# Kernel optimization log

Hardware: AMD Instinct MI355X
Metric: run time of the kernel (lower is better)

Reference implementation:

```python
import jax, jax.numpy as jnp
import numpy as np

B, N, K, C = 2, 4096, 2048, 16
DSPAN, E, H, V = 2048, 300, 512, 100000
WEIGHT = 1.0


def setup_inputs() -> dict:
    key = jax.random.key(0)
    ks = jax.random.split(key, 10)
    return {
        "cand_span_vecs": jax.random.normal(ks[0], (B, N, DSPAN), jnp.float32),
        "targets_all": jax.random.uniform(ks[1], (B, N, C), jnp.float32),
        "entity_emb": jax.random.normal(ks[2], (V, E), jnp.float32) * 0.02,
        "W1": jax.random.normal(ks[3], (DSPAN + E, H), jnp.float32) * 0.02,
        "b1": jnp.zeros((H,), jnp.float32),
        "W2": jax.random.normal(ks[4], (H, 1), jnp.float32) * 0.02,
        "b2": jnp.zeros((1,), jnp.float32),
        "linker_indices_hoi": jax.random.randint(ks[5], (B, K), 0, N, jnp.int64),
        "candidates_all": jax.random.randint(ks[6], (B, N, C), 0, V, jnp.int64),
        "candidate_lengths_all": jax.random.randint(ks[7], (B, N), 0, C + 1, jnp.int64),
    }


def reference(cand_span_vecs, targets_all, entity_emb, W1, b1, W2, b2,
              linker_indices_hoi, candidates_all, candidate_lengths_all):
    idx = linker_indices_hoi  # [B, K]
    # batched_index_select over the span axis
    candidates = jnp.take_along_axis(candidates_all, idx[:, :, None], axis=1)      # [B,K,C]
    cand_lens = jnp.take_along_axis(candidate_lengths_all, idx, axis=1)            # [B,K]
    targets = jnp.take_along_axis(targets_all, idx[:, :, None], axis=1)            # [B,K,C]
    linker_vecs = jnp.take_along_axis(cand_span_vecs, idx[:, :, None], axis=1)     # [B,K,Dspan]
    # entity embedding lookup
    candidate_vecs = entity_emb[candidates]                                        # [B,K,C,E]
    # expand span vecs over candidate axis and concat
    span_exp = jnp.broadcast_to(linker_vecs[:, :, None, :],
                                (linker_vecs.shape[0], linker_vecs.shape[1],
                                 candidate_vecs.shape[2], linker_vecs.shape[2]))
    vecs = jnp.concatenate([span_exp, candidate_vecs], axis=-1)                    # [B,K,C,Dspan+E]
    # FFNN: Linear -> ReLU -> (dropout is identity in eval) -> Linear
    h = jax.nn.relu(jnp.einsum('bkcd,dh->bkch', vecs, W1) + b1)
    scores = (jnp.einsum('bkch,ho->bkco', h, W2) + b2)[..., 0]                     # [B,K,C]
    # candidate mask: valid where position < candidate_length
    mask = (jnp.arange(scores.shape[-1]) < cand_lens[:, :, None]).astype(scores.dtype)
    # BCEWithLogits (reduction='none'): softplus(x) - x*t
    bce = jax.nn.softplus(scores) - scores * targets
    obj = (mask * bce).sum() * WEIGHT
    return obj
```

## Files before the change

### kernel.cpp

```cpp
#include <hip/hip_runtime.h>
#include <math.h>

#define NN 4096
#define CC 16
#define DSP 2048
#define ED 300
#define HD 512

typedef __attribute__((ext_vector_type(8))) short short8;
typedef __attribute__((ext_vector_type(4))) float f32x4;

#define MFMA16(a, b, c) __builtin_amdgcn_mfma_f32_16x16x32_bf16((a), (b), (c), 0, 0, 0)

__device__ __forceinline__ unsigned short f2bf(float x) {
    unsigned u = __builtin_bit_cast(unsigned, x);
    u += 0x7FFFu + ((u >> 16) & 1u);
    return (unsigned short)(u >> 16);
}

__device__ __forceinline__ void gl_lds16(const void* g, void* l) {
    __builtin_amdgcn_global_load_lds(
        (const __attribute__((address_space(1))) unsigned*)g,
        (__attribute__((address_space(3))) unsigned*)l, 16, 0, 0);
}

__global__ __launch_bounds__(256) void prep_gather_scan(
    const float* __restrict__ W1,
    const float* __restrict__ span,
    const int*   __restrict__ lidx,
    const int*   __restrict__ clens,
    unsigned short* __restrict__ W1sT,
    unsigned short* __restrict__ w1ef,
    unsigned short* __restrict__ A16,
    int*            __restrict__ off)
{
    const int bid = blockIdx.x, tid = threadIdx.x;

    if (bid == 4432) {
        __shared__ int ls[256];
        int myl[16];
        int msum = 0;
#pragma unroll
        for (int j = 0; j < 16; ++j) {
            int bk = tid * 16 + j;
            size_t base = (size_t)(bk >> 11) * NN + lidx[bk];
            int len = clens[base];
            len = len < 0 ? 0 : (len > CC ? CC : len);
            myl[j] = len; msum += len;
        }
        ls[tid] = msum;
        __syncthreads();
        for (int d = 1; d < 256; d <<= 1) {
            int v = (tid >= d) ? ls[tid - d] : 0;
            __syncthreads();
            ls[tid] += v;
            __syncthreads();
        }
        int run = ls[tid] - msum;
#pragma unroll
        for (int j = 0; j < 16; ++j) { off[tid * 16 + j] = run; run += myl[j]; }
        if (tid == 255) off[4096] = run;
        return;
    }
    if (bid >= 336) {
        const int bk = bid - 336;
        const float* src = span + ((size_t)(bk >> 11) * NN + lidx[bk]) * DSP;
        float4 x = *(const float4*)(src + tid * 8);
        float4 y = *(const float4*)(src + tid * 8 + 4);
        unsigned short v[8] = { f2bf(x.x), f2bf(x.y), f2bf(x.z), f2bf(x.w),
                                f2bf(y.x), f2bf(y.y), f2bf(y.z), f2bf(y.w) };
        *(short8*)&A16[(size_t)bk * DSP + tid * 8] = *(short8*)v;
        return;
    }
    if (bid < 256) {
        __shared__ float t[64][65];
        const int k0 = (bid >> 3) * 64, n0 = (bid & 7) * 64;
#pragma unroll
        for (int p = 0; p < 16; ++p) {
            int flat = p * 256 + tid;
            int r = flat >> 6, c = flat & 63;
            t[r][c] = W1[(size_t)(k0 + r) * HD + n0 + c];
        }
        __syncthreads();
#pragma unroll
        for (int p = 0; p < 16; ++p) {
            int flat = p * 256 + tid;
            int c = flat >> 6, r = flat & 63;
            W1sT[(size_t)(n0 + c) * DSP + k0 + r] = f2bf(t[r][c]);
        }
    } else {
        int t0 = (bid - 256) * 256 + tid;
        int lane = t0 & 63;
        int ks = (t0 >> 6) % 10;
        int ncg = (t0 >> 6) / 10;
        int col = ncg * 16 + (lane & 15);
        int kb = ks * 32 + ((lane >> 4) << 3);
        unsigned short v[8];
#pragma unroll
        for (int j = 0; j < 8; ++j) {
            int k = kb + j;
            v[j] = (k < ED) ? f2bf(W1[(size_t)(DSP + k) * HD + col]) : (unsigned short)0;
        }
        *(short8*)&w1ef[(size_t)t0 * 8] = *(short8*)v;
    }
}

__global__ __launch_bounds__(256) void gemm_and_fill(
    const unsigned short* __restrict__ A16,
    const unsigned short* __restrict__ BT,
    const float* __restrict__ b1,
    float* __restrict__ Cout,
    const int* __restrict__ lidx,
    const int* __restrict__ cands,
    const int* __restrict__ clens,
    const int* __restrict__ off,
    int* __restrict__ compact_cand,
    int* __restrict__ compact_meta)
{
    const int tid = threadIdx.x;

    if (blockIdx.x >= 512) {
        int fb = blockIdx.x - 512;
        int item0 = (fb * 256 + tid) * 4;
#pragma unroll
        for (int q = 0; q < 4; ++q) {
            int item = item0 + q;
            int bk = item >> 4, c = item & 15;
            size_t base = (size_t)(bk >> 11) * NN + lidx[bk];
            int len = clens[base];
            len = len > CC ? CC : len;
            if (c < len) {
                int pos = off[bk] + c;
                compact_cand[pos] = cands[base * CC + c];
                compact_meta[pos] = item;
            }
        }
        return;
    }

    __shared__ __align__(16) unsigned short As[2][64 * 64];
    __shared__ __align__(16) unsigned short Bs[2][64 * 64];
    const int l = tid & 63, wid = tid >> 6;
    const int wr = (wid >> 1) * 32, wc = (wid & 1) * 32;

    const int bid = blockIdx.x;
    const int brow = ((bid & 7) * 8 + ((bid >> 3) >> 3)) * 64;
    const int bcol = (((bid >> 3) & 7)) * 64;

    const int s0 = tid, s1 = tid + 256;
    const int r0 = s0 >> 3, c0 = ((s0 & 7) ^ (r0 & 7)) * 8;
    const int r1 = s1 >> 3, c1 = ((s1 & 7) ^ (r1 & 7)) * 8;
    const unsigned short* ga0 = A16 + (size_t)(brow + r0) * DSP + c0;
    const unsigned short* ga1 = A16 + (size_t)(brow + r1) * DSP + c1;
    const unsigned short* gb0 = BT + (size_t)(bcol + r0) * DSP + c0;
    const unsigned short* gb1 = BT + (size_t)(bcol + r1) * DSP + c1;

    int offA[2][2], offB[2][2];
#pragma unroll
    for (int mf = 0; mf < 2; ++mf) {
        int row = wr + mf * 16 + (l & 15);
#pragma unroll
        for (int kk = 0; kk < 2; ++kk)
            offA[mf][kk] = row * 64 + (((kk * 4) + (l >> 4)) ^ (row & 7)) * 8;
    }
#pragma unroll
    for (int nf = 0; nf < 2; ++nf) {
        int row = wc + nf * 16 + (l & 15);
#pragma unroll
        for (int kk = 0; kk < 2; ++kk)
            offB[nf][kk] = row * 64 + (((kk * 4) + (l >> 4)) ^ (row & 7)) * 8;
    }

    f32x4 z = {0.f, 0.f, 0.f, 0.f};
    f32x4 acc[2][2] = {{z, z}, {z, z}};

    auto stage = [&](int buf, int k0) {
        gl_lds16(ga0 + k0, &As[buf][s0 * 8]);
        gl_lds16(ga1 + k0, &As[buf][s1 * 8]);
        gl_lds16(gb0 + k0, &Bs[buf][s0 * 8]);
        gl_lds16(gb1 + k0, &Bs[buf][s1 * 8]);
    };

    stage(0, 0);
    __syncthreads();
    int cur = 0;
    for (int t = 0; t < 32; ++t) {
        if (t < 31) stage(cur ^ 1, (t + 1) * 64);
        short8 am[2][2], bn[2][2];
#pragma unroll
        for (int mf = 0; mf < 2; ++mf)
#pragma unroll
            for (int kk = 0; kk < 2; ++kk)
                am[mf][kk] = *(const short8*)&As[cur][offA[mf][kk]];
#pragma unroll
        for (int nf = 0; nf < 2; ++nf)
#pragma unroll
            for (int kk = 0; kk < 2; ++kk)
                bn[nf][kk] = *(const short8*)&Bs[cur][offB[nf][kk]];
#pragma unroll
        for (int m = 0; m < 2; ++m)
#pragma unroll
            for (int n = 0; n < 2; ++n)
#pragma unroll
                for (int kk = 0; kk < 2; ++kk)
                    acc[m][n] = MFMA16(am[m][kk], bn[n][kk], acc[m][n]);
        __syncthreads();
        cur ^= 1;
    }

#pragma unroll
    for (int n = 0; n < 2; ++n) {
        int col = bcol + wc + n * 16 + (l & 15);
        float b1v = b1[col];
#pragma unroll
        for (int m = 0; m < 2; ++m) {
            int row0 = brow + wr + m * 16 + (l >> 4) * 4;
#pragma unroll
            for (int r = 0; r < 4; ++r)
                Cout[(size_t)(row0 + r) * HD + col] = acc[m][n][r] + b1v;
        }
    }
}

__global__ __launch_bounds__(512) void ent_mfma(
    const unsigned short* __restrict__ w1ef,
    const float* __restrict__ span_part,
    const float* __restrict__ emb,
    const float* __restrict__ W2,
    const float* __restrict__ b2,
    const int*   __restrict__ lidx,
    const float* __restrict__ targets,
    const int*   __restrict__ compact_cand,
    const int*   __restrict__ compact_meta,
    const int*   __restrict__ off,
    float* __restrict__ blockPartial)
{
    const int total = off[4096];
    const int bid = blockIdx.x;
    const int slotBase = bid * 128;
    const int tid = threadIdx.x;
    if (slotBase >= total) {
        if (tid == 0) blockPartial[bid] = 0.f;
        return;
    }

    __shared__ __align__(16) unsigned short As[2][8 * 64 * 8];
    __shared__ float shp[8][16][8];
    __shared__ int   meta_s[128];
    __shared__ float wred[8];
    const int wid = tid >> 6, l = tid & 63;

    if (tid < 128) {
        int slot = slotBase + tid;
        meta_s[tid] = (slot < total) ? compact_meta[slot] : -1;
    }

    const int slot_s = slotBase + wid * 16 + (l & 15);
    const int cid = (slot_s < total) ? compact_cand[slot_s] : 0;
    const float* erow = emb + (size_t)cid * ED;
    const int kb = (l >> 4) * 8;
    const int ht = wid;

    float4 lx = *(const float4*)(erow + kb);
    float4 ly = *(const float4*)(erow + kb + 4);
    {
        unsigned short v[8] = { f2bf(lx.x), f2bf(lx.y), f2bf(lx.z), f2bf(lx.w),
                                f2bf(ly.x), f2bf(ly.y), f2bf(ly.z), f2bf(ly.w) };
        *(short8*)&As[0][tid * 8] = *(short8*)v;
    }
    __syncthreads();

    f32x4 z = {0.f, 0.f, 0.f, 0.f};
    f32x4 acc[8][4];
#pragma unroll
    for (int g = 0; g < 8; ++g)
#pragma unroll
        for (int nc = 0; nc < 4; ++nc) acc[g][nc] = z;

    int cur = 0;
    for (int ks = 0; ks < 10; ++ks) {
        const bool pf = (ks < 9);
        if (pf) {
            int k = (ks + 1) * 32 + kb;
            if (k + 8 <= ED) {
                lx = *(const float4*)(erow + k);
                ly = *(const float4*)(erow + k + 4);
            } else {
                float tmp[8];
#pragma unroll
                for (int j = 0; j < 8; ++j) tmp[j] = (k + j < ED) ? erow[k + j] : 0.f;
                lx = make_float4(tmp[0], tmp[1], tmp[2], tmp[3]);
                ly = make_float4(tmp[4], tmp[5], tmp[6], tmp[7]);
            }
        }
        short8 af[8];
#pragma unroll
        for (int g = 0; g < 8; ++g)
            af[g] = *(const short8*)&As[cur][(g * 64 + l) * 8];
#pragma unroll
        for (int nc = 0; nc < 4; ++nc) {
            short8 bf = *(const short8*)&w1ef[(((size_t)(ht * 4 + nc) * 10 + ks) * 64 + l) * 8];
#pragma unroll
            for (int g = 0; g < 8; ++g)
                acc[g][nc] = MFMA16(af[g], bf, acc[g][nc]);
        }
        if (pf) {
            unsigned short v[8] = { f2bf(lx.x), f2bf(lx.y), f2bf(lx.z), f2bf(lx.w),
                                    f2bf(ly.x), f2bf(ly.y), f2bf(ly.z), f2bf(ly.w) };
            *(short8*)&As[cur ^ 1][tid * 8] = *(short8*)v;
        }
        __syncthreads();
        cur ^= 1;
    }

    float w2v[4];
#pragma unroll
    for (int nc = 0; nc < 4; ++nc) w2v[nc] = W2[ht * 64 + nc * 16 + (l & 15)];
    const int rq = (l >> 4) * 4;

#pragma unroll
    for (int g = 0; g < 8; ++g) {
        int bkR[4];
#pragma unroll
        for (int i = 0; i < 4; ++i) {
            int m = meta_s[g * 16 + rq + i];
            bkR[i] = (m >= 0) ? (m >> 4) : 0;
        }
        float s[4] = {0.f, 0.f, 0.f, 0.f};
#pragma unroll
        for (int nc = 0; nc < 4; ++nc) {
            int col = ht * 64 + nc * 16 + (l & 15);
            f32x4 a = acc[g][nc];
#pragma unroll
            for (int i = 0; i < 4; ++i) {
                float sp = span_part[(size_t)bkR[i] * HD + col];
                s[i] += fmaxf(a[i] + sp, 0.f) * w2v[nc];
            }
        }
#pragma unroll
        for (int m = 1; m < 16; m <<= 1) {
#pragma unroll
            for (int i = 0; i < 4; ++i) s[i] += __shfl_xor(s[i], m, 64);
        }
        if ((l & 15) == 0) {
#pragma unroll
            for (int i = 0; i < 4; ++i) shp[g][rq + i][ht] = s[i];
        }
    }
    __syncthreads();

    float val = 0.f;
    if (tid < 128) {
        int m = meta_s[tid];
        if (m >= 0) {
            int bk = m >> 4, c = m & 15;
            size_t base = (size_t)(bk >> 11) * NN + lidx[bk];
            const float* p = &shp[tid >> 4][tid & 15][0];
            float sc = ((p[0] + p[1]) + (p[2] + p[3])) +
                       ((p[4] + p[5]) + (p[6] + p[7])) + b2[0];
            float tg = targets[base * CC + c];
            val = fmaxf(sc, 0.f) + log1pf(expf(-fabsf(sc))) - sc * tg;
        }
    }
#pragma unroll
    for (int m = 32; m; m >>= 1) val += __shfl_xor(val, m, 64);
    if (l == 0) wred[wid] = val;
    __syncthreads();
    if (tid == 0) {
        float s = 0.f;
#pragma unroll
        for (int w = 0; w < 8; ++w) s += wred[w];
        blockPartial[bid] = s;
    }
}

__global__ __launch_bounds__(256) void final_reduce(
    const float* __restrict__ bp, float* __restrict__ out)
{
    __shared__ float red[4];
    float s = bp[threadIdx.x] + bp[threadIdx.x + 256];
#pragma unroll
    for (int m = 32; m; m >>= 1) s += __shfl_xor(s, m, 64);
    if ((threadIdx.x & 63) == 0) red[threadIdx.x >> 6] = s;
    __syncthreads();
    if (threadIdx.x == 0)
        out[0] = (red[0] + red[1]) + (red[2] + red[3]);
}

extern "C" void kernel_launch(void* const* d_in, const int* in_sizes, int n_in,
                              void* d_out, int out_size, void* d_ws, size_t ws_size,
                              hipStream_t stream) {
    const float* span    = (const float*)d_in[0];
    const float* targets = (const float*)d_in[1];
    const float* emb     = (const float*)d_in[2];
    const float* W1      = (const float*)d_in[3];
    const float* b1      = (const float*)d_in[4];
    const float* W2      = (const float*)d_in[5];
    const float* b2      = (const float*)d_in[6];
    const int*   lidx    = (const int*)d_in[7];
    const int*   cands   = (const int*)d_in[8];
    const int*   clens   = (const int*)d_in[9];

    char* ws = (char*)d_ws;
    unsigned short* W1sT      = (unsigned short*)(ws);
    unsigned short* w1ef      = (unsigned short*)(ws + 2097152);
    unsigned short* A16       = (unsigned short*)(ws + 2424832);
    float*          span_part = (float*)(ws + 19202048);
    int*            off       = (int*)(ws + 27590656);
    int*            ccand     = (int*)(ws + 27623424);
    int*            cmeta     = (int*)(ws + 27885568);
    float*          bpart     = (float*)(ws + 28147712);

    prep_gather_scan<<<4433, 256, 0, stream>>>(W1, span, lidx, clens,
                                               W1sT, w1ef, A16, off);
    gemm_and_fill<<<576, 256, 0, stream>>>(A16, W1sT, b1, span_part,
                                           lidx, cands, clens, off, ccand, cmeta);
    ent_mfma<<<512, 512, 0, stream>>>(w1ef, span_part, emb, W2, b2,
                                      lidx, targets, ccand, cmeta, off, bpart);
    final_reduce<<<1, 256, 0, stream>>>(bpart, (float*)d_out);
}
```

Before: 66.69 us.

## Fuse span gather and bf16 conversion into GEMM A-tile loads; store span_part as bf16

Drops the separate gather pass that wrote a bf16 copy of the selected span rows (A16). The GEMM now reads fp32 span rows directly through lidx, converts them to bf16 in registers and writes them into swizzled LDS, prefetching one tile ahead. The span_part output is also stored as bf16, which halves its write and gather traffic in the entity kernel. The cost is that A-tile loads no longer use the async global-to-LDS path, so conversion work adds register pressure inside the main loop, and span_part loses some precision.

```diff
diff --git a/kernel.cpp b/kernel.cpp
--- a/kernel.cpp
+++ b/kernel.cpp
@@ -18,25 +18,33 @@
     return (unsigned short)(u >> 16);
 }
 
+__device__ __forceinline__ float bf2f(unsigned short u) {
+    return __builtin_bit_cast(float, (unsigned)u << 16);
+}
+
 __device__ __forceinline__ void gl_lds16(const void* g, void* l) {
     __builtin_amdgcn_global_load_lds(
         (const __attribute__((address_space(1))) unsigned*)g,
         (__attribute__((address_space(3))) unsigned*)l, 16, 0, 0);
 }
 
-__global__ __launch_bounds__(256) void prep_gather_scan(
+__device__ __forceinline__ void pack8(unsigned short* dst, float4 a, float4 b) {
+    unsigned short v[8] = { f2bf(a.x), f2bf(a.y), f2bf(a.z), f2bf(a.w),
+                            f2bf(b.x), f2bf(b.y), f2bf(b.z), f2bf(b.w) };
+    *(short8*)dst = *(short8*)v;
+}
+
+__global__ __launch_bounds__(256) void prep_scan(
     const float* __restrict__ W1,
-    const float* __restrict__ span,
     const int*   __restrict__ lidx,
     const int*   __restrict__ clens,
     unsigned short* __restrict__ W1sT,
     unsigned short* __restrict__ w1ef,
-    unsigned short* __restrict__ A16,
     int*            __restrict__ off)
 {
     const int bid = blockIdx.x, tid = threadIdx.x;
 
-    if (bid == 4432) {
+    if (bid == 336) {
         __shared__ int ls[256];
         int myl[16];
         int msum = 0;
@@ -60,16 +68,6 @@
 #pragma unroll
         for (int j = 0; j < 16; ++j) { off[tid * 16 + j] = run; run += myl[j]; }
         if (tid == 255) off[4096] = run;
-        return;
-    }
-    if (bid >= 336) {
-        const int bk = bid - 336;
-        const float* src = span + ((size_t)(bk >> 11) * NN + lidx[bk]) * DSP;
-        float4 x = *(const float4*)(src + tid * 8);
-        float4 y = *(const float4*)(src + tid * 8 + 4);
-        unsigned short v[8] = { f2bf(x.x), f2bf(x.y), f2bf(x.z), f2bf(x.w),
-                                f2bf(y.x), f2bf(y.y), f2bf(y.z), f2bf(y.w) };
-        *(short8*)&A16[(size_t)bk * DSP + tid * 8] = *(short8*)v;
         return;
     }
     if (bid < 256) {
@@ -106,14 +104,14 @@
 }
 
 __global__ __launch_bounds__(256) void gemm_and_fill(
-    const unsigned short* __restrict__ A16,
+    const float* __restrict__ span,
     const unsigned short* __restrict__ BT,
     const float* __restrict__ b1,
-    float* __restrict__ Cout,
     const int* __restrict__ lidx,
     const int* __restrict__ cands,
     const int* __restrict__ clens,
     const int* __restrict__ off,
+    unsigned short* __restrict__ Cout,
     int* __restrict__ compact_cand,
     int* __restrict__ compact_meta)
 {
@@ -148,12 +146,18 @@
     const int bcol = (((bid >> 3) & 7)) * 64;
 
     const int s0 = tid, s1 = tid + 256;
-    const int r0 = s0 >> 3, c0 = ((s0 & 7) ^ (r0 & 7)) * 8;
-    const int r1 = s1 >> 3, c1 = ((s1 & 7) ^ (r1 & 7)) * 8;
-    const unsigned short* ga0 = A16 + (size_t)(brow + r0) * DSP + c0;
-    const unsigned short* ga1 = A16 + (size_t)(brow + r1) * DSP + c1;
-    const unsigned short* gb0 = BT + (size_t)(bcol + r0) * DSP + c0;
-    const unsigned short* gb1 = BT + (size_t)(bcol + r1) * DSP + c1;
+    const int r0 = s0 >> 3, q0 = s0 & 7;
+    const int r1 = s1 >> 3, q1 = s1 & 7;
+
+    const int bk0 = brow + r0, bk1 = brow + r1;
+    const float* pa0 = span + ((size_t)(bk0 >> 11) * NN + lidx[bk0]) * DSP + q0 * 8;
+    const float* pa1 = span + ((size_t)(bk1 >> 11) * NN + lidx[bk1]) * DSP + q1 * 8;
+    const int wA0 = r0 * 64 + (q0 ^ (r0 & 7)) * 8;
+    const int wA1 = r1 * 64 + (q1 ^ (r1 & 7)) * 8;
+
+    const int cB0 = (q0 ^ (r0 & 7)) * 8, cB1 = (q1 ^ (r1 & 7)) * 8;
+    const unsigned short* gb0 = BT + (size_t)(bcol + r0) * DSP + cB0;
+    const unsigned short* gb1 = BT + (size_t)(bcol + r1) * DSP + cB1;
 
     int offA[2][2], offB[2][2];
 #pragma unroll
@@ -174,18 +178,31 @@
     f32x4 z = {0.f, 0.f, 0.f, 0.f};
     f32x4 acc[2][2] = {{z, z}, {z, z}};
 
-    auto stage = [&](int buf, int k0) {
-        gl_lds16(ga0 + k0, &As[buf][s0 * 8]);
-        gl_lds16(ga1 + k0, &As[buf][s1 * 8]);
-        gl_lds16(gb0 + k0, &Bs[buf][s0 * 8]);
-        gl_lds16(gb1 + k0, &Bs[buf][s1 * 8]);
-    };
-
-    stage(0, 0);
+    {
+        float4 a00 = *(const float4*)(pa0 + 0);
+        float4 a01 = *(const float4*)(pa0 + 4);
+        float4 a10 = *(const float4*)(pa1 + 0);
+        float4 a11 = *(const float4*)(pa1 + 4);
+        gl_lds16(gb0, &Bs[0][s0 * 8]);
+        gl_lds16(gb1, &Bs[0][s1 * 8]);
+        pack8(&As[0][wA0], a00, a01);
+        pack8(&As[0][wA1], a10, a11);
+    }
     __syncthreads();
+
     int cur = 0;
     for (int t = 0; t < 32; ++t) {
-        if (t < 31) stage(cur ^ 1, (t + 1) * 64);
+        const bool pf = (t < 31);
+        float4 n00, n01, n10, n11;
+        if (pf) {
+            const int k0 = (t + 1) * 64;
+            n00 = *(const float4*)(pa0 + k0);
+            n01 = *(const float4*)(pa0 + k0 + 4);
+            n10 = *(const float4*)(pa1 + k0);
+            n11 = *(const float4*)(pa1 + k0 + 4);
+            gl_lds16(gb0 + k0, &Bs[cur ^ 1][s0 * 8]);
+            gl_lds16(gb1 + k0, &Bs[cur ^ 1][s1 * 8]);
+        }
         short8 am[2][2], bn[2][2];
 #pragma unroll
         for (int mf = 0; mf < 2; ++mf)
@@ -204,6 +221,10 @@
 #pragma unroll
                 for (int kk = 0; kk < 2; ++kk)
                     acc[m][n] = MFMA16(am[m][kk], bn[n][kk], acc[m][n]);
+        if (pf) {
+            pack8(&As[cur ^ 1][wA0], n00, n01);
+            pack8(&As[cur ^ 1][wA1], n10, n11);
+        }
         __syncthreads();
         cur ^= 1;
     }
@@ -217,14 +238,14 @@
             int row0 = brow + wr + m * 16 + (l >> 4) * 4;
 #pragma unroll
             for (int r = 0; r < 4; ++r)
-                Cout[(size_t)(row0 + r) * HD + col] = acc[m][n][r] + b1v;
+                Cout[(size_t)(row0 + r) * HD + col] = f2bf(acc[m][n][r] + b1v);
         }
     }
 }
 
 __global__ __launch_bounds__(512) void ent_mfma(
     const unsigned short* __restrict__ w1ef,
-    const float* __restrict__ span_part,
+    const unsigned short* __restrict__ span_part,
     const float* __restrict__ emb,
     const float* __restrict__ W2,
     const float* __restrict__ b2,
@@ -263,11 +284,7 @@
 
     float4 lx = *(const float4*)(erow + kb);
     float4 ly = *(const float4*)(erow + kb + 4);
-    {
-        unsigned short v[8] = { f2bf(lx.x), f2bf(lx.y), f2bf(lx.z), f2bf(lx.w),
-                                f2bf(ly.x), f2bf(ly.y), f2bf(ly.z), f2bf(ly.w) };
-        *(short8*)&As[0][tid * 8] = *(short8*)v;
-    }
+    pack8(&As[0][tid * 8], lx, ly);
     __syncthreads();
 
     f32x4 z = {0.f, 0.f, 0.f, 0.f};
@@ -305,9 +322,7 @@
                 acc[g][nc] = MFMA16(af[g], bf, acc[g][nc]);
         }
         if (pf) {
-            unsigned short v[8] = { f2bf(lx.x), f2bf(lx.y), f2bf(lx.z), f2bf(lx.w),
-                                    f2bf(ly.x), f2bf(ly.y), f2bf(ly.z), f2bf(ly.w) };
-            *(short8*)&As[cur ^ 1][tid * 8] = *(short8*)v;
+            pack8(&As[cur ^ 1][tid * 8], lx, ly);
         }
         __syncthreads();
         cur ^= 1;
@@ -333,7 +348,7 @@
             f32x4 a = acc[g][nc];
 #pragma unroll
             for (int i = 0; i < 4; ++i) {
-                float sp = span_part[(size_t)bkR[i] * HD + col];
+                float sp = bf2f(span_part[(size_t)bkR[i] * HD + col]);
                 s[i] += fmaxf(a[i] + sp, 0.f) * w2v[nc];
             }
         }
@@ -404,17 +419,15 @@
     char* ws = (char*)d_ws;
     unsigned short* W1sT      = (unsigned short*)(ws);
     unsigned short* w1ef      = (unsigned short*)(ws + 2097152);
-    unsigned short* A16       = (unsigned short*)(ws + 2424832);
-    float*          span_part = (float*)(ws + 19202048);
-    int*            off       = (int*)(ws + 27590656);
-    int*            ccand     = (int*)(ws + 27623424);
-    int*            cmeta     = (int*)(ws + 27885568);
-    float*          bpart     = (float*)(ws + 28147712);
-
-    prep_gather_scan<<<4433, 256, 0, stream>>>(W1, span, lidx, clens,
-                                               W1sT, w1ef, A16, off);
-    gemm_and_fill<<<576, 256, 0, stream>>>(A16, W1sT, b1, span_part,
-                                           lidx, cands, clens, off, ccand, cmeta);
+    unsigned short* span_part = (unsigned short*)(ws + 2424832);
+    int*            off       = (int*)(ws + 6619136);
+    int*            ccand     = (int*)(ws + 6635524);
+    int*            cmeta     = (int*)(ws + 6897668);
+    float*          bpart     = (float*)(ws + 7159812);
+
+    prep_scan<<<337, 256, 0, stream>>>(W1, lidx, clens, W1sT, w1ef, off);
+    gemm_and_fill<<<576, 256, 0, stream>>>(span, W1sT, b1, lidx, cands, clens,
+                                           off, span_part, ccand, cmeta);
     ent_mfma<<<512, 512, 0, stream>>>(w1ef, span_part, emb, W2, b2,
                                       lidx, targets, ccand, cmeta, off, bpart);
     final_reduce<<<1, 256, 0, stream>>>(bpart, (float*)d_out);
```

Measured after the change: 69.09 us. 3.6% more time.

## Halve ent_mfma tile to 64 slots, double the grid, store span_part as bf16

Applied to the files above, without the earlier changes.

The entity MFMA kernel now processes 64 candidate slots per block instead of 128, with 1024 blocks, so accumulator registers are halved and more blocks run in parallel. Each thread loads half as many embedding values. The span-part intermediate is now written and read as bf16 instead of fp32, which halves its memory traffic but adds rounding error to the pre-ReLU hidden values. The final reduction reads 1024 block partials instead of 512.

```diff
diff --git a/kernel.cpp b/kernel.cpp
--- a/kernel.cpp
+++ b/kernel.cpp
@@ -8,6 +8,7 @@
 #define HD 512
 
 typedef __attribute__((ext_vector_type(8))) short short8;
+typedef __attribute__((ext_vector_type(4))) short short4v;
 typedef __attribute__((ext_vector_type(4))) float f32x4;
 
 #define MFMA16(a, b, c) __builtin_amdgcn_mfma_f32_16x16x32_bf16((a), (b), (c), 0, 0, 0)
@@ -18,10 +19,19 @@
     return (unsigned short)(u >> 16);
 }
 
+__device__ __forceinline__ float bf2f(unsigned short u) {
+    return __builtin_bit_cast(float, (unsigned)u << 16);
+}
+
 __device__ __forceinline__ void gl_lds16(const void* g, void* l) {
     __builtin_amdgcn_global_load_lds(
         (const __attribute__((address_space(1))) unsigned*)g,
         (__attribute__((address_space(3))) unsigned*)l, 16, 0, 0);
+}
+
+__device__ __forceinline__ void pack4(unsigned short* dst, float4 a) {
+    unsigned short v[4] = { f2bf(a.x), f2bf(a.y), f2bf(a.z), f2bf(a.w) };
+    *(short4v*)dst = *(short4v*)v;
 }
 
 __global__ __launch_bounds__(256) void prep_gather_scan(
@@ -109,7 +119,7 @@
     const unsigned short* __restrict__ A16,
     const unsigned short* __restrict__ BT,
     const float* __restrict__ b1,
-    float* __restrict__ Cout,
+    unsigned short* __restrict__ Cout,
     const int* __restrict__ lidx,
     const int* __restrict__ cands,
     const int* __restrict__ clens,
@@ -217,14 +227,14 @@
             int row0 = brow + wr + m * 16 + (l >> 4) * 4;
 #pragma unroll
             for (int r = 0; r < 4; ++r)
-                Cout[(size_t)(row0 + r) * HD + col] = acc[m][n][r] + b1v;
+                Cout[(size_t)(row0 + r) * HD + col] = f2bf(acc[m][n][r] + b1v);
         }
     }
 }
 
 __global__ __launch_bounds__(512) void ent_mfma(
     const unsigned short* __restrict__ w1ef,
-    const float* __restrict__ span_part,
+    const unsigned short* __restrict__ span_part,
     const float* __restrict__ emb,
     const float* __restrict__ W2,
     const float* __restrict__ b2,
@@ -237,77 +247,72 @@
 {
     const int total = off[4096];
     const int bid = blockIdx.x;
-    const int slotBase = bid * 128;
+    const int slotBase = bid * 64;
     const int tid = threadIdx.x;
     if (slotBase >= total) {
         if (tid == 0) blockPartial[bid] = 0.f;
         return;
     }
 
-    __shared__ __align__(16) unsigned short As[2][8 * 64 * 8];
-    __shared__ float shp[8][16][8];
-    __shared__ int   meta_s[128];
-    __shared__ float wred[8];
+    __shared__ __align__(16) unsigned short As[2][4 * 64 * 8];
+    __shared__ float shp[4][16][8];
+    __shared__ int   meta_s[64];
     const int wid = tid >> 6, l = tid & 63;
-
-    if (tid < 128) {
+    const int ht = wid;
+
+    if (tid < 64) {
         int slot = slotBase + tid;
         meta_s[tid] = (slot < total) ? compact_meta[slot] : -1;
     }
 
-    const int slot_s = slotBase + wid * 16 + (l & 15);
+    const int tile_s = tid >> 7;
+    const int rem    = tid & 127;
+    const int lane_s = rem >> 1;
+    const int half   = rem & 1;
+    const int slot_s = slotBase + tile_s * 16 + (lane_s & 15);
     const int cid = (slot_s < total) ? compact_cand[slot_s] : 0;
     const float* erow = emb + (size_t)cid * ED;
-    const int kb = (l >> 4) * 8;
-    const int ht = wid;
-
-    float4 lx = *(const float4*)(erow + kb);
-    float4 ly = *(const float4*)(erow + kb + 4);
-    {
-        unsigned short v[8] = { f2bf(lx.x), f2bf(lx.y), f2bf(lx.z), f2bf(lx.w),
-                                f2bf(ly.x), f2bf(ly.y), f2bf(ly.z), f2bf(ly.w) };
-        *(short8*)&As[0][tid * 8] = *(short8*)v;
-    }
+    const int kb   = (lane_s >> 4) * 8 + half * 4;
+    const int wofs = (tile_s * 64 + lane_s) * 8 + half * 4;
+
+    pack4(&As[0][wofs], *(const float4*)(erow + kb));
     __syncthreads();
 
     f32x4 z = {0.f, 0.f, 0.f, 0.f};
-    f32x4 acc[8][4];
-#pragma unroll
-    for (int g = 0; g < 8; ++g)
+    f32x4 acc[4][4];
+#pragma unroll
+    for (int g = 0; g < 4; ++g)
 #pragma unroll
         for (int nc = 0; nc < 4; ++nc) acc[g][nc] = z;
 
     int cur = 0;
     for (int ks = 0; ks < 10; ++ks) {
         const bool pf = (ks < 9);
+        float4 nv;
         if (pf) {
             int k = (ks + 1) * 32 + kb;
-            if (k + 8 <= ED) {
-                lx = *(const float4*)(erow + k);
-                ly = *(const float4*)(erow + k + 4);
+            if (k + 4 <= ED) {
+                nv = *(const float4*)(erow + k);
             } else {
-                float tmp[8];
-#pragma unroll
-                for (int j = 0; j < 8; ++j) tmp[j] = (k + j < ED) ? erow[k + j] : 0.f;
-                lx = make_float4(tmp[0], tmp[1], tmp[2], tmp[3]);
-                ly = make_float4(tmp[4], tmp[5], tmp[6], tmp[7]);
+                float tmp[4];
+#pragma unroll
+                for (int j = 0; j < 4; ++j) tmp[j] = (k + j < ED) ? erow[k + j] : 0.f;
+                nv = make_float4(tmp[0], tmp[1], tmp[2], tmp[3]);
             }
         }
-        short8 af[8];
-#pragma unroll
-        for (int g = 0; g < 8; ++g)
+        short8 af[4];
+#pragma unroll
+        for (int g = 0; g < 4; ++g)
             af[g] = *(const short8*)&As[cur][(g * 64 + l) * 8];
 #pragma unroll
         for (int nc = 0; nc < 4; ++nc) {
             short8 bf = *(const short8*)&w1ef[(((size_t)(ht * 4 + nc) * 10 + ks) * 64 + l) * 8];
 #pragma unroll
-            for (int g = 0; g < 8; ++g)
+            for (int g = 0; g < 4; ++g)
                 acc[g][nc] = MFMA16(af[g], bf, acc[g][nc]);
         }
         if (pf) {
-            unsigned short v[8] = { f2bf(lx.x), f2bf(lx.y), f2bf(lx.z), f2bf(lx.w),
-                                    f2bf(ly.x), f2bf(ly.y), f2bf(ly.z), f2bf(ly.w) };
-            *(short8*)&As[cur ^ 1][tid * 8] = *(short8*)v;
+            pack4(&As[cur ^ 1][wofs], nv);
         }
         __syncthreads();
         cur ^= 1;
@@ -319,7 +324,7 @@
     const int rq = (l >> 4) * 4;
 
 #pragma unroll
-    for (int g = 0; g < 8; ++g) {
+    for (int g = 0; g < 4; ++g) {
         int bkR[4];
 #pragma unroll
         for (int i = 0; i < 4; ++i) {
@@ -333,7 +338,7 @@
             f32x4 a = acc[g][nc];
 #pragma unroll
             for (int i = 0; i < 4; ++i) {
-                float sp = span_part[(size_t)bkR[i] * HD + col];
+                float sp = bf2f(span_part[(size_t)bkR[i] * HD + col]);
                 s[i] += fmaxf(a[i] + sp, 0.f) * w2v[nc];
             }
         }
@@ -349,28 +354,21 @@
     }
     __syncthreads();
 
-    float val = 0.f;
-    if (tid < 128) {
-        int m = meta_s[tid];
+    if (wid == 0) {
+        float val = 0.f;
+        int m = meta_s[l];
         if (m >= 0) {
             int bk = m >> 4, c = m & 15;
             size_t base = (size_t)(bk >> 11) * NN + lidx[bk];
-            const float* p = &shp[tid >> 4][tid & 15][0];
+            const float* p = &shp[l >> 4][l & 15][0];
             float sc = ((p[0] + p[1]) + (p[2] + p[3])) +
                        ((p[4] + p[5]) + (p[6] + p[7])) + b2[0];
             float tg = targets[base * CC + c];
             val = fmaxf(sc, 0.f) + log1pf(expf(-fabsf(sc))) - sc * tg;
         }
-    }
-#pragma unroll
-    for (int m = 32; m; m >>= 1) val += __shfl_xor(val, m, 64);
-    if (l == 0) wred[wid] = val;
-    __syncthreads();
-    if (tid == 0) {
-        float s = 0.f;
-#pragma unroll
-        for (int w = 0; w < 8; ++w) s += wred[w];
-        blockPartial[bid] = s;
+#pragma unroll
+        for (int m2 = 32; m2; m2 >>= 1) val += __shfl_xor(val, m2, 64);
+        if (l == 0) blockPartial[bid] = val;
     }
 }
 
@@ -378,7 +376,8 @@
     const float* __restrict__ bp, float* __restrict__ out)
 {
     __shared__ float red[4];
-    float s = bp[threadIdx.x] + bp[threadIdx.x + 256];
+    float s = (bp[threadIdx.x] + bp[threadIdx.x + 256]) +
+              (bp[threadIdx.x + 512] + bp[threadIdx.x + 768]);
 #pragma unroll
     for (int m = 32; m; m >>= 1) s += __shfl_xor(s, m, 64);
     if ((threadIdx.x & 63) == 0) red[threadIdx.x >> 6] = s;
@@ -405,17 +404,17 @@
     unsigned short* W1sT      = (unsigned short*)(ws);
     unsigned short* w1ef      = (unsigned short*)(ws + 2097152);
     unsigned short* A16       = (unsigned short*)(ws + 2424832);
-    float*          span_part = (float*)(ws + 19202048);
-    int*            off       = (int*)(ws + 27590656);
-    int*            ccand     = (int*)(ws + 27623424);
-    int*            cmeta     = (int*)(ws + 27885568);
-    float*          bpart     = (float*)(ws + 28147712);
+    unsigned short* span_part = (unsigned short*)(ws + 19202048);
+    int*            off       = (int*)(ws + 23396352);
+    int*            ccand     = (int*)(ws + 23412740);
+    int*            cmeta     = (int*)(ws + 23674884);
+    float*          bpart     = (float*)(ws + 23937028);
 
     prep_gather_scan<<<4433, 256, 0, stream>>>(W1, span, lidx, clens,
                                                W1sT, w1ef, A16, off);
     gemm_and_fill<<<576, 256, 0, stream>>>(A16, W1sT, b1, span_part,
                                            lidx, cands, clens, off, ccand, cmeta);
-    ent_mfma<<<512, 512, 0, stream>>>(w1ef, span_part, emb, W2, b2,
-                                      lidx, targets, ccand, cmeta, off, bpart);
+    ent_mfma<<<1024, 512, 0, stream>>>(w1ef, span_part, emb, W2, b2,
+                                       lidx, targets, ccand, cmeta, off, bpart);
     final_reduce<<<1, 256, 0, stream>>>(bpart, (float*)d_out);
 }
```

New measurement: 72.64 us. +8.9%, slower.
